# Kernel optimization log

Measured on AMD Instinct MI355X. Metric: run time of the kernel, lower is better.

The kernel has to match this reference:

```python
import jax, jax.numpy as jnp
import numpy as np

N = 100000   # nodes
E = 1600000  # edges
F = 128      # feature dim == Dense units
R = 50       # relations
BN_EPS = 1e-3  # keras BatchNormalization default epsilon


def setup_inputs() -> dict:
    key = jax.random.key(0)
    ks = jax.random.split(key, 8)
    x = jax.random.normal(ks[0], (N, F), dtype=jnp.float32)
    edge_rows = jax.random.randint(ks[1], (E,), 0, N, dtype=jnp.int32)
    edge_cols = jax.random.randint(ks[2], (E,), 0, N, dtype=jnp.int32)
    edge_vals = jax.random.uniform(ks[3], (E,), dtype=jnp.float32)
    rel_ids = jax.random.randint(ks[4], (E,), 0, R, dtype=jnp.int32)
    relation_coeffs = jax.random.uniform(ks[5], (R,), dtype=jnp.float32)
    coeff_kernel = jax.random.normal(ks[6], (N, 1), dtype=jnp.float32) * 0.05
    dense_kernel = jax.random.normal(ks[7], (F, F), dtype=jnp.float32) / np.sqrt(F).astype(np.float32)
    dense_bias = jnp.zeros((F,), dtype=jnp.float32)
    bn_gamma = jnp.ones((F,), dtype=jnp.float32)
    bn_beta = jnp.zeros((F,), dtype=jnp.float32)
    bn_mean = jnp.zeros((F,), dtype=jnp.float32)
    bn_var = jnp.ones((F,), dtype=jnp.float32)
    return {
        "x": x, "edge_rows": edge_rows, "edge_cols": edge_cols,
        "edge_vals": edge_vals, "rel_ids": rel_ids,
        "relation_coeffs": relation_coeffs, "coeff_kernel": coeff_kernel,
        "dense_kernel": dense_kernel, "dense_bias": dense_bias,
        "bn_gamma": bn_gamma, "bn_beta": bn_beta,
        "bn_mean": bn_mean, "bn_var": bn_var,
    }


def reference(x, edge_rows, edge_cols, edge_vals, rel_ids,
              relation_coeffs, coeff_kernel, dense_kernel, dense_bias,
              bn_gamma, bn_beta, bn_mean, bn_var):
    # BatchNorm (inference: moving statistics)
    h = (x - bn_mean) * jax.lax.rsqrt(bn_var + BN_EPS) * bn_gamma + bn_beta  # [N, F]
    # relation_coeff_adj2: edge weight = A.values * (rel_coeffs[rel] + 1)^-1
    w = edge_vals / (relation_coeffs[rel_ids] + 1.0)  # [E]
    # SpMM: out[i] = sum_{(i,j) in edges} w_e * h[j]
    msgs = w[:, None] * h[edge_cols]                   # [E, F]
    agg = jax.ops.segment_sum(msgs, edge_rows, num_segments=N)  # [N, F]
    # CoeffLayer(mul=True): inputs * (kernel + 1)
    pre = agg + h * (coeff_kernel + 1.0)               # [N, F]
    # Dense
    return pre @ dense_kernel + dense_bias             # [N, F]
```

## Files before the change

kernel.cpp:

```cpp
#include <hip/hip_runtime.h>
#include <stdint.h>

#define N_NODES 100000
#define N_EDGES 1600000
#define FDIM 128
#define NREL 50
#define BN_EPS 1e-3f
#define N_PAD 100096
#define NBUCK 782
#define EPB 8192
#define NBLK 196
#define NSEG 4
#define SLACK 384
#define HBLK 6250

typedef short short8_t __attribute__((ext_vector_type(8)));
typedef float f32x4_t __attribute__((ext_vector_type(4)));

__device__ __forceinline__ uint32_t f2bf(float f) {
    union { float f; uint32_t u; } v; v.f = f;
    uint32_t u = v.u;
    return (u + 0x7FFFu + ((u >> 16) & 1u)) >> 16;
}
__device__ __forceinline__ float bflo(uint32_t p) {
    union { uint32_t u; float f; } v; v.u = p << 16; return v.f;
}
__device__ __forceinline__ float bfhi(uint32_t p) {
    union { uint32_t u; float f; } v; v.u = p & 0xFFFF0000u; return v.f;
}

__global__ __launch_bounds__(512) void pre_kernel(
        const float* __restrict__ x, const int* __restrict__ rows,
        const float* __restrict__ gamma, const float* __restrict__ beta,
        const float* __restrict__ mean, const float* __restrict__ var,
        const float* __restrict__ W,
        uint2* __restrict__ h, int* __restrict__ bhist, uint16_t* __restrict__ WT) {
    __shared__ int lh[NBUCK];
    int b = blockIdx.x, t = threadIdx.x;
    if (b < NBLK) {
        for (int i = t; i < NBUCK; i += 512) lh[i] = 0;
        __syncthreads();
        int e0 = b * EPB, e1 = min(e0 + EPB, N_EDGES);
        for (int e = e0 + t; e < e1; e += 512)
            atomicAdd(&lh[rows[e] >> 7], 1);
        __syncthreads();
        for (int i = t; i < NBUCK; i += 512) bhist[(size_t)i * NBLK + b] = lh[i];
    } else if (b == NBLK) {
        for (int idx = t; idx < FDIM * FDIM; idx += 512) {
            int f = idx >> 7, k = idx & 127;
            WT[idx] = (uint16_t)f2bf(W[k * FDIM + f]);
        }
    } else {
        int i4 = (b - NBLK - 1) * 512 + t;
        int cg = (i4 & 31) * 4;
        float4 xv = ((const float4*)x)[i4];
        float4 g4 = *(const float4*)(gamma + cg);
        float4 b4 = *(const float4*)(beta + cg);
        float4 m4 = *(const float4*)(mean + cg);
        float4 v4 = *(const float4*)(var + cg);
        float s0 = g4.x * rsqrtf(v4.x + BN_EPS);
        float s1 = g4.y * rsqrtf(v4.y + BN_EPS);
        float s2 = g4.z * rsqrtf(v4.z + BN_EPS);
        float s3 = g4.w * rsqrtf(v4.w + BN_EPS);
        uint2 o;
        o.x = f2bf((xv.x - m4.x) * s0 + b4.x) | (f2bf((xv.y - m4.y) * s1 + b4.y) << 16);
        o.y = f2bf((xv.z - m4.z) * s2 + b4.z) | (f2bf((xv.w - m4.w) * s3 + b4.w) << 16);
        h[i4] = o;
    }
}

__global__ __launch_bounds__(256) void btot_kernel(const int* __restrict__ bhist,
                                                   int* __restrict__ btot) {
    int wv = (blockIdx.x * 256 + threadIdx.x) >> 6;
    int lane = threadIdx.x & 63;
    if (wv >= NBUCK) return;
    int s = 0;
    for (int idx = lane; idx < NBLK; idx += 64) s += bhist[(size_t)wv * NBLK + idx];
    for (int d = 32; d > 0; d >>= 1) s += __shfl_down(s, d);
    if (lane == 0) btot[wv] = s;
}

__global__ __launch_bounds__(1024) void bprefix_kernel(const int* __restrict__ btot,
                                                       int* __restrict__ bstart) {
    __shared__ int sm[1024];
    int t = threadIdx.x;
    int v = (t < NBUCK) ? btot[t] : 0;
    sm[t] = v;
    __syncthreads();
    for (int off = 1; off < 1024; off <<= 1) {
        int xv = (t >= off) ? sm[t - off] : 0;
        __syncthreads();
        sm[t] += xv;
        __syncthreads();
    }
    if (t < NBUCK) bstart[t] = sm[t] - v;
    if (t == 0) bstart[NBUCK] = sm[1023];
}

__global__ __launch_bounds__(256) void bscan_kernel(const int* __restrict__ bhist,
                                                    const int* __restrict__ bstart,
                                                    int* __restrict__ bbase) {
    int wv = (blockIdx.x * 256 + threadIdx.x) >> 6;
    int lane = threadIdx.x & 63;
    if (wv >= NBUCK) return;
    int base = bstart[wv];
    int carry = 0;
#pragma unroll
    for (int seg = 0; seg < NSEG; ++seg) {
        int idx = seg * 64 + lane;
        int v = (idx < NBLK) ? bhist[(size_t)wv * NBLK + idx] : 0;
        int s = v;
        for (int d = 1; d < 64; d <<= 1) {
            int u = __shfl_up(s, d);
            if (lane >= d) s += u;
        }
        if (idx < NBLK) bbase[(size_t)wv * NBLK + idx] = base + carry + s - v;
        carry += __shfl(s, 63);
    }
}

__global__ __launch_bounds__(1024) void sort2_kernel(
        const int* __restrict__ rows, const int* __restrict__ cols,
        const float* __restrict__ vals, const int* __restrict__ rels,
        const float* __restrict__ relc, const int* __restrict__ bbase,
        uint2* __restrict__ staging) {
    __shared__ int lcur[NBUCK];
    __shared__ float lrel[NREL];
    int t = threadIdx.x, b = blockIdx.x;
    if (t < NREL) lrel[t] = 1.0f / (relc[t] + 1.0f);
    for (int i = t; i < NBUCK; i += 1024) lcur[i] = bbase[(size_t)i * NBLK + b];
    __syncthreads();
    int e0 = b * EPB, e1 = min(e0 + EPB, N_EDGES);
    for (int e = e0 + t; e < e1; e += 1024) {
        int r = rows[e];
        float w = vals[e] * lrel[rels[e]];
        int p = atomicAdd(&lcur[r >> 7], 1);
        uint2 s;
        s.x = (uint32_t)cols[e] | ((uint32_t)(r & 127) << 20);
        s.y = __float_as_uint(w);
        staging[p] = s;
    }
}

__global__ __launch_bounds__(256) void bucket_kernel(
        const uint2* __restrict__ staging, const int* __restrict__ bstart,
        uint2* __restrict__ rowrange, uint2* __restrict__ scolw) {
    __shared__ int lh[128];
    __shared__ int sm[128];
    __shared__ int lcur[128];
    int b = blockIdx.x, r0 = b << 7, t = threadIdx.x;
    int nrows = min(128, N_NODES - r0);
    if (t < 128) lh[t] = 0;
    __syncthreads();
    int e0 = bstart[b], e1 = bstart[b + 1];
    for (int e = e0 + t; e < e1; e += 256)
        atomicAdd(&lh[(staging[e].x >> 20) & 127], 1);
    __syncthreads();
    int v = (t < 128) ? lh[t] : 0;
    int pv = (v + 3) & ~3;
    if (t < 128) sm[t] = pv;
    __syncthreads();
    for (int off = 1; off < 128; off <<= 1) {
        int xv = 0;
        if (t < 128 && t >= off) xv = sm[t - off];
        __syncthreads();
        if (t < 128) sm[t] += xv;
        __syncthreads();
    }
    int sbase = e0 + SLACK * b;
    int start = 0;
    if (t < 128) {
        start = sbase + sm[t] - pv;
        lcur[t] = start;
        if (t < nrows) {
            uint2 rr; rr.x = (uint32_t)start; rr.y = (uint32_t)(start + pv);
            rowrange[r0 + t] = rr;
        }
    }
    __syncthreads();
    for (int e = e0 + t; e < e1; e += 256) {
        uint2 s = staging[e];
        int rl = (s.x >> 20) & 127;
        int p = atomicAdd(&lcur[rl], 1);
        uint2 o; o.x = s.x & 0xFFFFF; o.y = s.y;
        scolw[p] = o;
    }
    if (t < 128) {
        uint2 z; z.x = 0; z.y = 0;
        for (int k = v; k < pv; ++k) scolw[start + k] = z;
    }
}

__global__ __launch_bounds__(256) void spmm_kernel(
        const uint32_t* __restrict__ h, const uint2* __restrict__ rowrange,
        const uint2* __restrict__ scolw, const float* __restrict__ ck,
        uint32_t* __restrict__ pre) {
    int row = blockIdx.x * 4 + (threadIdx.x >> 6);
    int lane = threadIdx.x & 63;
    uint2 rr = rowrange[row];
    int e  = __builtin_amdgcn_readfirstlane((int)rr.x);
    int e1 = __builtin_amdgcn_readfirstlane((int)rr.y);
    uint32_t p = h[(size_t)row * 64 + lane];
    float coef = ck[row] + 1.0f;
    float ax = coef * bflo(p);
    float ay = coef * bfhi(p);
    for (; e < e1; e += 4) {
        const uint4* ep = (const uint4*)(scolw + e);
        uint4 eA = ep[0];
        uint4 eB = ep[1];
        uint32_t q0 = h[eA.x * 64u + lane];
        uint32_t q1 = h[eA.z * 64u + lane];
        uint32_t q2 = h[eB.x * 64u + lane];
        uint32_t q3 = h[eB.z * 64u + lane];
        float w0 = __uint_as_float(eA.y), w1 = __uint_as_float(eA.w);
        float w2 = __uint_as_float(eB.y), w3 = __uint_as_float(eB.w);
        ax += w0 * bflo(q0); ay += w0 * bfhi(q0);
        ax += w1 * bflo(q1); ay += w1 * bfhi(q1);
        ax += w2 * bflo(q2); ay += w2 * bfhi(q2);
        ax += w3 * bflo(q3); ay += w3 * bfhi(q3);
    }
    pre[(size_t)row * 64 + lane] = f2bf(ax) | (f2bf(ay) << 16);
}

__global__ __launch_bounds__(256) void gemm_kernel(
        const uint16_t* __restrict__ pre, const uint16_t* __restrict__ WT,
        const float* __restrict__ bias, float* __restrict__ out) {
    int wave = threadIdx.x >> 6;
    int lane = threadIdx.x & 63;
    int row0 = blockIdx.x * 64 + wave * 16;
    int m = lane & 15, q = lane >> 4;

    short8_t a[4];
    const uint16_t* arow = pre + (size_t)(row0 + m) * FDIM + q * 8;
#pragma unroll
    for (int t = 0; t < 4; ++t)
        a[t] = *(const short8_t*)(arow + t * 32);

    for (int ct = 0; ct < 8; ++ct) {
        int col0 = ct * 16;
        const uint16_t* brow = WT + (size_t)(col0 + m) * FDIM + q * 8;
        f32x4_t acc = {0.f, 0.f, 0.f, 0.f};
#pragma unroll
        for (int t = 0; t < 4; ++t) {
            short8_t b = *(const short8_t*)(brow + t * 32);
            acc = __builtin_amdgcn_mfma_f32_16x16x32_bf16(a[t], b, acc, 0, 0, 0);
        }
        float bs = bias[col0 + m];
#pragma unroll
        for (int r = 0; r < 4; ++r) {
            int row = row0 + q * 4 + r;
            if (row < N_NODES)
                out[(size_t)row * FDIM + col0 + m] = acc[r] + bs;
        }
    }
}

extern "C" void kernel_launch(void* const* d_in, const int* in_sizes, int n_in,
                              void* d_out, int out_size, void* d_ws, size_t ws_size,
                              hipStream_t stream) {
    const float* x     = (const float*)d_in[0];
    const int*   erows = (const int*)d_in[1];
    const int*   ecols = (const int*)d_in[2];
    const float* evals = (const float*)d_in[3];
    const int*   erels = (const int*)d_in[4];
    const float* relc  = (const float*)d_in[5];
    const float* ck    = (const float*)d_in[6];
    const float* W     = (const float*)d_in[7];
    const float* bias  = (const float*)d_in[8];
    const float* gamma = (const float*)d_in[9];
    const float* beta  = (const float*)d_in[10];
    const float* mean  = (const float*)d_in[11];
    const float* var   = (const float*)d_in[12];
    float* out = (float*)d_out;

    char* wp = (char*)d_ws;
    auto alloc = [&](size_t bytes) {
        char* p = wp;
        wp += (bytes + 255) & ~(size_t)255;
        return (void*)p;
    };
    uint16_t* h      = (uint16_t*)alloc((size_t)N_PAD * FDIM * 2);
    uint16_t* pre    = (uint16_t*)alloc((size_t)N_PAD * FDIM * 2);
    uint2* scolw     = (uint2*)alloc((size_t)(N_EDGES + SLACK * NBUCK) * 8);
    uint2* rowrange  = (uint2*)alloc((size_t)N_NODES * 8);
    int* bhist       = (int*)alloc((size_t)NBUCK * NBLK * 4);
    int* bbase       = (int*)alloc((size_t)NBUCK * NBLK * 4);
    int* btot        = (int*)alloc((size_t)NBUCK * 4);
    int* bstart      = (int*)alloc((size_t)(NBUCK + 1) * 4);
    uint16_t* WT     = (uint16_t*)alloc(FDIM * FDIM * 2);
    if ((size_t)(wp - (char*)d_ws) > ws_size) return;

    uint2* staging = (uint2*)pre;

    pre_kernel<<<NBLK + 1 + HBLK, 512, 0, stream>>>(x, erows, gamma, beta, mean, var, W,
                                                    (uint2*)h, bhist, WT);
    btot_kernel<<<(NBUCK + 3) / 4, 256, 0, stream>>>(bhist, btot);
    bprefix_kernel<<<1, 1024, 0, stream>>>(btot, bstart);
    bscan_kernel<<<(NBUCK + 3) / 4, 256, 0, stream>>>(bhist, bstart, bbase);
    sort2_kernel<<<NBLK, 1024, 0, stream>>>(erows, ecols, evals, erels, relc, bbase, staging);
    bucket_kernel<<<NBUCK, 256, 0, stream>>>(staging, bstart, rowrange, scolw);
    spmm_kernel<<<N_NODES / 4, 256, 0, stream>>>((const uint32_t*)h, rowrange, scolw, ck,
                                                 (uint32_t*)pre);
    gemm_kernel<<<(N_NODES + 63) / 64, 256, 0, stream>>>(pre, WT, bias, out);
}
```

Measured before the change: 287.4 us.

## Collapse sort pipeline into atomic bucket claim and fuse SpMM with GEMM

```diff
diff --git a/kernel.cpp b/kernel.cpp
--- a/kernel.cpp
+++ b/kernel.cpp
@@ -10,9 +10,10 @@
 #define NBUCK 782
 #define EPB 8192
 #define NBLK 196
-#define NSEG 4
-#define SLACK 384
 #define HBLK 6250
+#define LEDCAP 2816
+#define SCAP 3712
+#define NSG 1563
 
 typedef short short8_t __attribute__((ext_vector_type(8)));
 typedef float f32x4_t __attribute__((ext_vector_type(4)));
@@ -31,20 +32,39 @@
 
 __global__ __launch_bounds__(512) void pre_kernel(
         const float* __restrict__ x, const int* __restrict__ rows,
+        const int* __restrict__ cols, const float* __restrict__ vals,
+        const int* __restrict__ rels, const float* __restrict__ relc,
         const float* __restrict__ gamma, const float* __restrict__ beta,
         const float* __restrict__ mean, const float* __restrict__ var,
         const float* __restrict__ W,
-        uint2* __restrict__ h, int* __restrict__ bhist, uint16_t* __restrict__ WT) {
+        uint2* __restrict__ h, uint16_t* __restrict__ WT,
+        int* __restrict__ gcur, uint2* __restrict__ staging) {
     __shared__ int lh[NBUCK];
+    __shared__ float lrel[NREL];
     int b = blockIdx.x, t = threadIdx.x;
     if (b < NBLK) {
+        if (t < NREL) lrel[t] = 1.0f / (relc[t] + 1.0f);
         for (int i = t; i < NBUCK; i += 512) lh[i] = 0;
         __syncthreads();
         int e0 = b * EPB, e1 = min(e0 + EPB, N_EDGES);
         for (int e = e0 + t; e < e1; e += 512)
             atomicAdd(&lh[rows[e] >> 7], 1);
         __syncthreads();
-        for (int i = t; i < NBUCK; i += 512) bhist[(size_t)i * NBLK + b] = lh[i];
+        for (int i = t; i < NBUCK; i += 512) {
+            int c = lh[i];
+            int base = c ? atomicAdd(&gcur[i], c) : 0;
+            lh[i] = i * SCAP + base;
+        }
+        __syncthreads();
+        for (int e = e0 + t; e < e1; e += 512) {
+            int r = rows[e];
+            float w = vals[e] * lrel[rels[e]];
+            int p = atomicAdd(&lh[r >> 7], 1);
+            uint2 s;
+            s.x = (uint32_t)cols[e] | ((uint32_t)(r & 127) << 20);
+            s.y = __float_as_uint(w);
+            staging[p] = s;
+        }
     } else if (b == NBLK) {
         for (int idx = t; idx < FDIM * FDIM; idx += 512) {
             int f = idx >> 7, k = idx & 127;
@@ -69,95 +89,27 @@
     }
 }
 
-__global__ __launch_bounds__(256) void btot_kernel(const int* __restrict__ bhist,
-                                                   int* __restrict__ btot) {
-    int wv = (blockIdx.x * 256 + threadIdx.x) >> 6;
-    int lane = threadIdx.x & 63;
-    if (wv >= NBUCK) return;
-    int s = 0;
-    for (int idx = lane; idx < NBLK; idx += 64) s += bhist[(size_t)wv * NBLK + idx];
-    for (int d = 32; d > 0; d >>= 1) s += __shfl_down(s, d);
-    if (lane == 0) btot[wv] = s;
-}
-
-__global__ __launch_bounds__(1024) void bprefix_kernel(const int* __restrict__ btot,
-                                                       int* __restrict__ bstart) {
-    __shared__ int sm[1024];
-    int t = threadIdx.x;
-    int v = (t < NBUCK) ? btot[t] : 0;
-    sm[t] = v;
-    __syncthreads();
-    for (int off = 1; off < 1024; off <<= 1) {
-        int xv = (t >= off) ? sm[t - off] : 0;
-        __syncthreads();
-        sm[t] += xv;
-        __syncthreads();
-    }
-    if (t < NBUCK) bstart[t] = sm[t] - v;
-    if (t == 0) bstart[NBUCK] = sm[1023];
-}
-
-__global__ __launch_bounds__(256) void bscan_kernel(const int* __restrict__ bhist,
-                                                    const int* __restrict__ bstart,
-                                                    int* __restrict__ bbase) {
-    int wv = (blockIdx.x * 256 + threadIdx.x) >> 6;
-    int lane = threadIdx.x & 63;
-    if (wv >= NBUCK) return;
-    int base = bstart[wv];
-    int carry = 0;
-#pragma unroll
-    for (int seg = 0; seg < NSEG; ++seg) {
-        int idx = seg * 64 + lane;
-        int v = (idx < NBLK) ? bhist[(size_t)wv * NBLK + idx] : 0;
-        int s = v;
-        for (int d = 1; d < 64; d <<= 1) {
-            int u = __shfl_up(s, d);
-            if (lane >= d) s += u;
-        }
-        if (idx < NBLK) bbase[(size_t)wv * NBLK + idx] = base + carry + s - v;
-        carry += __shfl(s, 63);
-    }
-}
-
-__global__ __launch_bounds__(1024) void sort2_kernel(
-        const int* __restrict__ rows, const int* __restrict__ cols,
-        const float* __restrict__ vals, const int* __restrict__ rels,
-        const float* __restrict__ relc, const int* __restrict__ bbase,
-        uint2* __restrict__ staging) {
-    __shared__ int lcur[NBUCK];
-    __shared__ float lrel[NREL];
-    int t = threadIdx.x, b = blockIdx.x;
-    if (t < NREL) lrel[t] = 1.0f / (relc[t] + 1.0f);
-    for (int i = t; i < NBUCK; i += 1024) lcur[i] = bbase[(size_t)i * NBLK + b];
-    __syncthreads();
-    int e0 = b * EPB, e1 = min(e0 + EPB, N_EDGES);
-    for (int e = e0 + t; e < e1; e += 1024) {
-        int r = rows[e];
-        float w = vals[e] * lrel[rels[e]];
-        int p = atomicAdd(&lcur[r >> 7], 1);
-        uint2 s;
-        s.x = (uint32_t)cols[e] | ((uint32_t)(r & 127) << 20);
-        s.y = __float_as_uint(w);
-        staging[p] = s;
-    }
-}
-
 __global__ __launch_bounds__(256) void bucket_kernel(
-        const uint2* __restrict__ staging, const int* __restrict__ bstart,
-        uint2* __restrict__ rowrange, uint2* __restrict__ scolw) {
+        const int* __restrict__ gcur, uint2* __restrict__ staging,
+        uint2* __restrict__ rowrange) {
+    __shared__ uint2 led[LEDCAP];
     __shared__ int lh[128];
     __shared__ int sm[128];
     __shared__ int lcur[128];
     int b = blockIdx.x, r0 = b << 7, t = threadIdx.x;
     int nrows = min(128, N_NODES - r0);
+    int cnt = min(gcur[b], LEDCAP);
+    uint2* sg = staging + (size_t)b * SCAP;
     if (t < 128) lh[t] = 0;
     __syncthreads();
-    int e0 = bstart[b], e1 = bstart[b + 1];
-    for (int e = e0 + t; e < e1; e += 256)
-        atomicAdd(&lh[(staging[e].x >> 20) & 127], 1);
+    for (int e = t; e < cnt; e += 256) {
+        uint2 s = sg[e];
+        led[e] = s;
+        atomicAdd(&lh[(s.x >> 20) & 127], 1);
+    }
     __syncthreads();
     int v = (t < 128) ? lh[t] : 0;
-    int pv = (v + 3) & ~3;
+    int pv = (v + 7) & ~7;
     if (t < 128) sm[t] = pv;
     __syncthreads();
     for (int off = 1; off < 128; off <<= 1) {
@@ -167,7 +119,7 @@
         if (t < 128) sm[t] += xv;
         __syncthreads();
     }
-    int sbase = e0 + SLACK * b;
+    int sbase = b * SCAP;
     int start = 0;
     if (t < 128) {
         start = sbase + sm[t] - pv;
@@ -178,77 +130,93 @@
         }
     }
     __syncthreads();
-    for (int e = e0 + t; e < e1; e += 256) {
-        uint2 s = staging[e];
+    for (int e = t; e < cnt; e += 256) {
+        uint2 s = led[e];
         int rl = (s.x >> 20) & 127;
         int p = atomicAdd(&lcur[rl], 1);
         uint2 o; o.x = s.x & 0xFFFFF; o.y = s.y;
-        scolw[p] = o;
+        staging[p] = o;
     }
     if (t < 128) {
         uint2 z; z.x = 0; z.y = 0;
-        for (int k = v; k < pv; ++k) scolw[start + k] = z;
-    }
-}
-
-__global__ __launch_bounds__(256) void spmm_kernel(
+        for (int k = v; k < pv; ++k) staging[start + k] = z;
+    }
+}
+
+__global__ __launch_bounds__(256, 6) void sg_kernel(
         const uint32_t* __restrict__ h, const uint2* __restrict__ rowrange,
         const uint2* __restrict__ scolw, const float* __restrict__ ck,
-        uint32_t* __restrict__ pre) {
-    int row = blockIdx.x * 4 + (threadIdx.x >> 6);
+        const uint16_t* __restrict__ WT, const float* __restrict__ bias,
+        float* __restrict__ out) {
+    __shared__ uint32_t lp[64 * 64];
+    int wv = threadIdx.x >> 6;
     int lane = threadIdx.x & 63;
-    uint2 rr = rowrange[row];
-    int e  = __builtin_amdgcn_readfirstlane((int)rr.x);
-    int e1 = __builtin_amdgcn_readfirstlane((int)rr.y);
-    uint32_t p = h[(size_t)row * 64 + lane];
-    float coef = ck[row] + 1.0f;
-    float ax = coef * bflo(p);
-    float ay = coef * bfhi(p);
-    for (; e < e1; e += 4) {
-        const uint4* ep = (const uint4*)(scolw + e);
-        uint4 eA = ep[0];
-        uint4 eB = ep[1];
-        uint32_t q0 = h[eA.x * 64u + lane];
-        uint32_t q1 = h[eA.z * 64u + lane];
-        uint32_t q2 = h[eB.x * 64u + lane];
-        uint32_t q3 = h[eB.z * 64u + lane];
-        float w0 = __uint_as_float(eA.y), w1 = __uint_as_float(eA.w);
-        float w2 = __uint_as_float(eB.y), w3 = __uint_as_float(eB.w);
-        ax += w0 * bflo(q0); ay += w0 * bfhi(q0);
-        ax += w1 * bflo(q1); ay += w1 * bfhi(q1);
-        ax += w2 * bflo(q2); ay += w2 * bfhi(q2);
-        ax += w3 * bflo(q3); ay += w3 * bfhi(q3);
-    }
-    pre[(size_t)row * 64 + lane] = f2bf(ax) | (f2bf(ay) << 16);
-}
-
-__global__ __launch_bounds__(256) void gemm_kernel(
-        const uint16_t* __restrict__ pre, const uint16_t* __restrict__ WT,
-        const float* __restrict__ bias, float* __restrict__ out) {
-    int wave = threadIdx.x >> 6;
-    int lane = threadIdx.x & 63;
-    int row0 = blockIdx.x * 64 + wave * 16;
+    int row0 = blockIdx.x * 64;
+
+    for (int ri = 0; ri < 16; ++ri) {
+        int rl = wv * 16 + ri;
+        int row = row0 + rl;
+        float ax = 0.f, ay = 0.f;
+        if (row < N_NODES) {
+            uint2 rg = rowrange[row];
+            int e  = __builtin_amdgcn_readfirstlane((int)rg.x);
+            int e1 = __builtin_amdgcn_readfirstlane((int)rg.y);
+            uint32_t p = h[(uint32_t)row * 64u + lane];
+            float coef = ck[row] + 1.0f;
+            ax = coef * bflo(p);
+            ay = coef * bfhi(p);
+            for (; e < e1; e += 8) {
+                const uint4* ep = (const uint4*)(scolw + e);
+                uint4 eA = ep[0], eB = ep[1], eC = ep[2], eD = ep[3];
+                uint32_t q0 = h[eA.x * 64u + lane];
+                uint32_t q1 = h[eA.z * 64u + lane];
+                uint32_t q2 = h[eB.x * 64u + lane];
+                uint32_t q3 = h[eB.z * 64u + lane];
+                uint32_t q4 = h[eC.x * 64u + lane];
+                uint32_t q5 = h[eC.z * 64u + lane];
+                uint32_t q6 = h[eD.x * 64u + lane];
+                uint32_t q7 = h[eD.z * 64u + lane];
+                float w0 = __uint_as_float(eA.y), w1 = __uint_as_float(eA.w);
+                float w2 = __uint_as_float(eB.y), w3 = __uint_as_float(eB.w);
+                float w4 = __uint_as_float(eC.y), w5 = __uint_as_float(eC.w);
+                float w6 = __uint_as_float(eD.y), w7 = __uint_as_float(eD.w);
+                ax += w0 * bflo(q0); ay += w0 * bfhi(q0);
+                ax += w1 * bflo(q1); ay += w1 * bfhi(q1);
+                ax += w2 * bflo(q2); ay += w2 * bfhi(q2);
+                ax += w3 * bflo(q3); ay += w3 * bfhi(q3);
+                ax += w4 * bflo(q4); ay += w4 * bfhi(q4);
+                ax += w5 * bflo(q5); ay += w5 * bfhi(q5);
+                ax += w6 * bflo(q6); ay += w6 * bfhi(q6);
+                ax += w7 * bflo(q7); ay += w7 * bfhi(q7);
+            }
+        }
+        uint32_t pk = f2bf(ax) | (f2bf(ay) << 16);
+        lp[rl * 64 + (lane ^ ((rl & 7) << 2))] = pk;
+    }
+    __syncthreads();
+
     int m = lane & 15, q = lane >> 4;
-
+    int rowm = wv * 16 + m;
     short8_t a[4];
-    const uint16_t* arow = pre + (size_t)(row0 + m) * FDIM + q * 8;
 #pragma unroll
-    for (int t = 0; t < 4; ++t)
-        a[t] = *(const short8_t*)(arow + t * 32);
-
+    for (int t = 0; t < 4; ++t) {
+        int w0 = (q * 4 + t * 16) ^ ((rowm & 7) << 2);
+        a[t] = *(const short8_t*)&lp[rowm * 64 + w0];
+    }
+    int row0m = row0 + wv * 16;
     for (int ct = 0; ct < 8; ++ct) {
         int col0 = ct * 16;
         const uint16_t* brow = WT + (size_t)(col0 + m) * FDIM + q * 8;
         f32x4_t acc = {0.f, 0.f, 0.f, 0.f};
 #pragma unroll
         for (int t = 0; t < 4; ++t) {
-            short8_t b = *(const short8_t*)(brow + t * 32);
-            acc = __builtin_amdgcn_mfma_f32_16x16x32_bf16(a[t], b, acc, 0, 0, 0);
+            short8_t bb = *(const short8_t*)(brow + t * 32);
+            acc = __builtin_amdgcn_mfma_f32_16x16x32_bf16(a[t], bb, acc, 0, 0, 0);
         }
         float bs = bias[col0 + m];
 #pragma unroll
         for (int r = 0; r < 4; ++r) {
-            int row = row0 + q * 4 + r;
+            int row = row0m + q * 4 + r;
             if (row < N_NODES)
                 out[(size_t)row * FDIM + col0 + m] = acc[r] + bs;
         }
@@ -280,26 +248,17 @@
         return (void*)p;
     };
     uint16_t* h      = (uint16_t*)alloc((size_t)N_PAD * FDIM * 2);
-    uint16_t* pre    = (uint16_t*)alloc((size_t)N_PAD * FDIM * 2);
-    uint2* scolw     = (uint2*)alloc((size_t)(N_EDGES + SLACK * NBUCK) * 8);
-    uint2* rowrange  = (uint2*)alloc((size_t)N_NODES * 8);
-    int* bhist       = (int*)alloc((size_t)NBUCK * NBLK * 4);
-    int* bbase       = (int*)alloc((size_t)NBUCK * NBLK * 4);
-    int* btot        = (int*)alloc((size_t)NBUCK * 4);
-    int* bstart      = (int*)alloc((size_t)(NBUCK + 1) * 4);
+    uint2* staging   = (uint2*)alloc((size_t)NBUCK * SCAP * 8);
+    uint2* rowrange  = (uint2*)alloc((size_t)N_PAD * 8);
+    int* gcur        = (int*)alloc((size_t)NBUCK * 4);
     uint16_t* WT     = (uint16_t*)alloc(FDIM * FDIM * 2);
     if ((size_t)(wp - (char*)d_ws) > ws_size) return;
 
-    uint2* staging = (uint2*)pre;
-
-    pre_kernel<<<NBLK + 1 + HBLK, 512, 0, stream>>>(x, erows, gamma, beta, mean, var, W,
-                                                    (uint2*)h, bhist, WT);
-    btot_kernel<<<(NBUCK + 3) / 4, 256, 0, stream>>>(bhist, btot);
-    bprefix_kernel<<<1, 1024, 0, stream>>>(btot, bstart);
-    bscan_kernel<<<(NBUCK + 3) / 4, 256, 0, stream>>>(bhist, bstart, bbase);
-    sort2_kernel<<<NBLK, 1024, 0, stream>>>(erows, ecols, evals, erels, relc, bbase, staging);
-    bucket_kernel<<<NBUCK, 256, 0, stream>>>(staging, bstart, rowrange, scolw);
-    spmm_kernel<<<N_NODES / 4, 256, 0, stream>>>((const uint32_t*)h, rowrange, scolw, ck,
-                                                 (uint32_t*)pre);
-    gemm_kernel<<<(N_NODES + 63) / 64, 256, 0, stream>>>(pre, WT, bias, out);
-}
+    hipMemsetAsync(gcur, 0, (size_t)NBUCK * 4, stream);
+    pre_kernel<<<NBLK + 1 + HBLK, 512, 0, stream>>>(
+        x, erows, ecols, evals, erels, relc, gamma, beta, mean, var, W,
+        (uint2*)h, WT, gcur, staging);
+    bucket_kernel<<<NBUCK, 256, 0, stream>>>(gcur, staging, rowrange);
+    sg_kernel<<<NSG, 256, 0, stream>>>((const uint32_t*)h, rowrange, staging, ck,
+                                       WT, bias, out);
+}
```

Result: faster. 270.7 us (-5.8%).
